# Performance work log

Measured on AMD Instinct MI355X. Metric: run time of the kernel, lower is better.

The kernel has to match this reference:

```python
import jax, jax.numpy as jnp
import numpy as np

NUM_OPS = 8
D = 1024
B = 8192


def setup_inputs() -> dict:
    key = jax.random.key(0)
    k1, k2, k3, k4 = jax.random.split(key, 4)
    x = jax.random.normal(k1, (B, D), dtype=jnp.float32)
    logits = 0.001 * jax.random.normal(k2, (NUM_OPS,), dtype=jnp.float32)
    Ws = jax.random.normal(k3, (NUM_OPS, D, D), dtype=jnp.float32) * (1.0 / np.sqrt(D))
    bs = jax.random.normal(k4, (NUM_OPS, D), dtype=jnp.float32) * 0.01
    return {"x": x, "logits": logits, "Ws": Ws, "bs": bs, "num_on_samples": 2}


def reference(x, logits, Ws, bs, num_on_samples):
    # non_stochastic_call: top-k op selection by architecture logits,
    # dispatch x to the selected ops, sum-combine the results.
    _, top_k_ids = jax.lax.top_k(logits, num_on_samples)  # [k]
    W_sel = jnp.take(Ws, top_k_ids, axis=0)  # [k, D, D]
    b_sel = jnp.take(bs, top_k_ids, axis=0)  # [k, D]
    # each op is Dense(D->D) + relu: [k, B, D]
    op_results = jax.nn.relu(jnp.einsum('bd,kde->kbe', x, W_sel) + b_sel[:, None, :])
    return jnp.sum(op_results, axis=0)  # [B, D]
```

## Files before the change

### kernel.cpp

```cpp
#include <hip/hip_runtime.h>
#include <hip/hip_bf16.h>

#define NUM_OPS 8
#define D 1024
#define B_ROWS 8192

typedef unsigned short ushort_t;
typedef __attribute__((ext_vector_type(8))) short bf16x8;
typedef __attribute__((ext_vector_type(4))) float f32x4;
typedef __attribute__((ext_vector_type(4))) float float4v;
typedef __attribute__((ext_vector_type(8))) unsigned short ushort8;

__device__ __forceinline__ unsigned short f2bf(float f) {
    union { float f; unsigned int u; } v; v.f = f;
    unsigned int u = v.u;
    unsigned int lsb = (u >> 16) & 1u;
    u += 0x7fffu + lsb;
    return (unsigned short)(u >> 16);
}

__device__ __forceinline__ void load_lds16(const void* g, void* l) {
    __builtin_amdgcn_global_load_lds(
        (const __attribute__((address_space(1))) void*)g,
        (__attribute__((address_space(3))) void*)l,
        16, 0, 0);
}

__device__ __forceinline__ void top2(const float* __restrict__ logits, int& i0, int& i1) {
    float best = -__builtin_inff(); i0 = 0;
    for (int i = 0; i < NUM_OPS; ++i) { float v = logits[i]; if (v > best) { best = v; i0 = i; } }
    float best2 = -__builtin_inff(); i1 = 0;
    for (int i = 0; i < NUM_OPS; ++i) {
        if (i == i0) continue;
        float v = logits[i]; if (v > best2) { best2 = v; i1 = i; }
    }
}

__global__ void prep_kernel(const float* __restrict__ x,
                            const float* __restrict__ Ws,
                            const float* __restrict__ logits,
                            ushort_t* __restrict__ xbf,
                            ushort_t* __restrict__ Wt) {
    __shared__ float t[32][33];
    const int bid = blockIdx.x;
    const int tid = threadIdx.x;
    if (bid < 4096) {
        int i = (bid * 256 + tid) * 8;
        float4v v0 = *(const float4v*)(x + i);
        float4v v1 = *(const float4v*)(x + i + 4);
        ushort8 o;
        o[0] = f2bf(v0[0]); o[1] = f2bf(v0[1]); o[2] = f2bf(v0[2]); o[3] = f2bf(v0[3]);
        o[4] = f2bf(v1[0]); o[5] = f2bf(v1[1]); o[6] = f2bf(v1[2]); o[7] = f2bf(v1[3]);
        *(ushort8*)(xbf + i) = o;
    } else {
        int i0, i1; top2(logits, i0, i1);
        const int b  = bid - 4096;
        const int e    = b >> 10;
        const int tile = b & 1023;
        const int td = (tile >> 5) << 5;
        const int te = (tile & 31) << 5;
        const int tx = tid & 31, ty = tid >> 5;
        const float* W = Ws + (size_t)(e ? i1 : i0) * D * D;
        for (int r = 0; r < 4; ++r)
            t[ty + 8 * r][tx] = W[(size_t)(td + ty + 8 * r) * D + te + tx];
        __syncthreads();
        ushort_t* o = Wt + (size_t)e * D * D;
        for (int r = 0; r < 4; ++r)
            o[(size_t)(te + ty + 8 * r) * D + td + tx] = f2bf(t[tx][ty + 8 * r]);
    }
}

__device__ __forceinline__ void stageA(const ushort_t* __restrict__ xbf, int brow,
                                       int u, ushort_t* dst, int tid) {
    #pragma unroll
    for (int q = 0; q < 4; ++q) {
        const int c   = q * 512 + tid;
        const int rr  = c >> 3;
        const int gcb = ((c & 7) * 16) ^ ((rr & 7) << 4);
        load_lds16(xbf + (size_t)(brow + rr) * D + u * 64 + (gcb >> 1), dst + c * 8);
    }
}
__device__ __forceinline__ void stageB(const ushort_t* __restrict__ Wt, int bcol,
                                       int u, ushort_t* dst, int tid) {
    #pragma unroll
    for (int q = 0; q < 2; ++q) {
        const int c   = q * 512 + tid;
        const int e   = c >> 9, cc = c & 511;
        const int n   = cc >> 3;
        const int gcb = ((cc & 7) * 16) ^ ((n & 7) << 4);
        load_lds16(Wt + (size_t)e * D * D + (size_t)(bcol + n) * D + u * 64 + (gcb >> 1),
                   dst + c * 8);
    }
}

#define SB()    __builtin_amdgcn_sched_barrier(0)
#define PRIO1() __builtin_amdgcn_s_setprio(1)
#define PRIO0() __builtin_amdgcn_s_setprio(0)
#define VMW(N)  do { asm volatile("s_waitcnt vmcnt(" #N ")" ::: "memory"); SB(); } while (0)
#define LGW(N)  do { asm volatile("s_waitcnt lgkmcnt(" #N ")" ::: "memory"); SB(); } while (0)
#define BAR()   do { __builtin_amdgcn_s_barrier(); SB(); } while (0)

#define DSR(dst, addr, imm)                                                    \
    asm volatile("ds_read_b128 %0, %1 offset:" #imm : "=v"(dst) : "v"(addr))

#define ISSUE_DS(P, SA, SBB)                                                   \
    do {                                                                       \
        unsigned aA0 = (unsigned)(size_t)(SA) + aro + x0;                      \
        unsigned aA1 = (unsigned)(size_t)(SA) + aro + x1;                      \
        unsigned aB0 = (unsigned)(size_t)(SBB) + bro + x0;                     \
        unsigned aB1 = (unsigned)(size_t)(SBB) + bro + x1;                     \
        DSR(P##a0, aA0, 0);    DSR(P##a1, aA0, 2048);                          \
        DSR(P##a2, aA0, 4096); DSR(P##a3, aA0, 6144);                          \
        DSR(P##a4, aA1, 0);    DSR(P##a5, aA1, 2048);                          \
        DSR(P##a6, aA1, 4096); DSR(P##a7, aA1, 6144);                          \
        DSR(P##b0, aB0, 0);    DSR(P##b1, aB0, 2048);                          \
        DSR(P##b4, aB0, 8192); DSR(P##b5, aB0, 10240);                         \
        DSR(P##b2, aB1, 0);    DSR(P##b3, aB1, 2048);                          \
        DSR(P##b6, aB1, 8192); DSR(P##b7, aB1, 10240);                         \
    } while (0)

#define MF(a, b, c) __builtin_amdgcn_mfma_f32_16x16x32_bf16(a, b, c, 0, 0, 0)
#define Q(P, A, B, E, M, N) acc[E][M][N] = MF(P##A, P##B, acc[E][M][N])

#define MFMA_SET(P)                                                            \
    do {                                                                       \
        PRIO1();                                                               \
        Q(P,a0,b0,0,0,0); Q(P,a0,b1,0,0,1); Q(P,a0,b4,1,0,0); Q(P,a0,b5,1,0,1);\
        Q(P,a1,b0,0,1,0); Q(P,a1,b1,0,1,1); Q(P,a1,b4,1,1,0); Q(P,a1,b5,1,1,1);\
        Q(P,a2,b0,0,2,0); Q(P,a2,b1,0,2,1); Q(P,a2,b4,1,2,0); Q(P,a2,b5,1,2,1);\
        Q(P,a3,b0,0,3,0); Q(P,a3,b1,0,3,1); Q(P,a3,b4,1,3,0); Q(P,a3,b5,1,3,1);\
        Q(P,a4,b2,0,0,0); Q(P,a4,b3,0,0,1); Q(P,a4,b6,1,0,0); Q(P,a4,b7,1,0,1);\
        Q(P,a5,b2,0,1,0); Q(P,a5,b3,0,1,1); Q(P,a5,b6,1,1,0); Q(P,a5,b7,1,1,1);\
        Q(P,a6,b2,0,2,0); Q(P,a6,b3,0,2,1); Q(P,a6,b6,1,2,0); Q(P,a6,b7,1,2,1);\
        Q(P,a7,b2,0,3,0); Q(P,a7,b3,0,3,1); Q(P,a7,b6,1,3,0); Q(P,a7,b7,1,3,1);\
        PRIO0();                                                               \
    } while (0)

#define TILE(SETN, SA, SBB, SU, DA, DB, SETC, DOSTG)                           \
    do {                                                                       \
        VMW(0);                                                                \
        BAR();                                                                 \
        ISSUE_DS(SETN, SA, SBB);                                               \
        if (DOSTG) { stageA(xbf, brow, (SU), DA, tid);                         \
                     stageB(Wt,  bcol, (SU), DB, tid); }                       \
        SB();                                                                  \
        LGW(15);                                                               \
        MFMA_SET(SETC);                                                        \
        SB();                                                                  \
    } while (0)

__global__ __launch_bounds__(512, 2)
void gemm_dual(const ushort_t* __restrict__ xbf, const ushort_t* __restrict__ Wt,
               const float* __restrict__ bs, const float* __restrict__ logits,
               float* __restrict__ out) {
    __shared__ __align__(16) ushort_t As0[256 * 64], As1[256 * 64], As2[256 * 64];
    __shared__ __align__(16) ushort_t Bs0[2 * 64 * 64], Bs1[2 * 64 * 64], Bs2[2 * 64 * 64];

    const int tid  = threadIdx.x;
    const int wv   = tid >> 6;
    const int lane = tid & 63;
    const int rgrp = wv >> 1, cgrp = wv & 1;
    const int l15  = lane & 15, lq = lane >> 4;
    const int swz  = (l15 & 7) << 4;
    const int x0   = (lq * 16) ^ swz;
    const int x1   = (64 + lq * 16) ^ swz;
    const unsigned aro = (unsigned)((rgrp * 64 + l15) * 128);
    const unsigned bro = (unsigned)((cgrp * 32 + l15) * 128);

    const int bid  = blockIdx.x;
    const int brow = (bid & 31) * 256;
    const int bcol = (bid >> 5) * 64;

    f32x4 acc[2][4][2] = {};

    bf16x8 Xa0, Xa1, Xa2, Xa3, Xa4, Xa5, Xa6, Xa7;
    bf16x8 Xb0, Xb1, Xb2, Xb3, Xb4, Xb5, Xb6, Xb7;
    bf16x8 Ya0, Ya1, Ya2, Ya3, Ya4, Ya5, Ya6, Ya7;
    bf16x8 Yb0, Yb1, Yb2, Yb3, Yb4, Yb5, Yb6, Yb7;

    stageA(xbf, brow, 0, As0, tid); stageB(Wt, bcol, 0, Bs0, tid);
    stageA(xbf, brow, 1, As1, tid); stageB(Wt, bcol, 1, Bs1, tid);
    SB();
    VMW(6);
    BAR();
    ISSUE_DS(X, As0, Bs0);
    SB();

    TILE(Y, As1, Bs1,  2, As2, Bs2, X, true);
    TILE(X, As2, Bs2,  3, As0, Bs0, Y, true);
    TILE(Y, As0, Bs0,  4, As1, Bs1, X, true);
    TILE(X, As1, Bs1,  5, As2, Bs2, Y, true);
    TILE(Y, As2, Bs2,  6, As0, Bs0, X, true);
    TILE(X, As0, Bs0,  7, As1, Bs1, Y, true);
    TILE(Y, As1, Bs1,  8, As2, Bs2, X, true);
    TILE(X, As2, Bs2,  9, As0, Bs0, Y, true);
    TILE(Y, As0, Bs0, 10, As1, Bs1, X, true);
    TILE(X, As1, Bs1, 11, As2, Bs2, Y, true);
    TILE(Y, As2, Bs2, 12, As0, Bs0, X, true);
    TILE(X, As0, Bs0, 13, As1, Bs1, Y, true);
    TILE(Y, As1, Bs1, 14, As2, Bs2, X, true);
    TILE(X, As2, Bs2, 15, As0, Bs0, Y, true);
    TILE(Y, As0, Bs0,  0, As0, Bs0, X, false);
    LGW(0);
    MFMA_SET(Y);
    SB();

    int i0, i1; top2(logits, i0, i1);
    #pragma unroll
    for (int n16 = 0; n16 < 2; ++n16) {
        const int col = bcol + cgrp * 32 + n16 * 16 + l15;
        const float bb0 = bs[i0 * D + col];
        const float bb1 = bs[i1 * D + col];
        #pragma unroll
        for (int m = 0; m < 4; ++m) {
            const int rbase = brow + rgrp * 64 + m * 16 + lq * 4;
            #pragma unroll
            for (int i = 0; i < 4; ++i) {
                float v0 = acc[0][m][n16][i] + bb0; v0 = v0 > 0.f ? v0 : 0.f;
                float v1 = acc[1][m][n16][i] + bb1; v1 = v1 > 0.f ? v1 : 0.f;
                out[(size_t)(rbase + i) * D + col] = v0 + v1;
            }
        }
    }
}

extern "C" void kernel_launch(void* const* d_in, const int* in_sizes, int n_in,
                              void* d_out, int out_size, void* d_ws, size_t ws_size,
                              hipStream_t stream) {
    const float* x      = (const float*)d_in[0];
    const float* logits = (const float*)d_in[1];
    const float* Ws     = (const float*)d_in[2];
    const float* bs     = (const float*)d_in[3];
    float* out = (float*)d_out;

    char* ws = (char*)d_ws;
    ushort_t* xbf = (ushort_t*)ws;
    ushort_t* Wt  = (ushort_t*)(ws + (size_t)B_ROWS * D * 2);

    prep_kernel<<<4096 + 2048, 256, 0, stream>>>(x, Ws, logits, xbf, Wt);
    gemm_dual<<<512, 512, 0, stream>>>(xbf, Wt, bs, logits, out);
}
```

Before: 49.06 us.

## Deepen global-to-LDS prefetch to two tiles ahead with partial vmcnt waits

Prologue now stages three K-tiles instead of two. Each iteration waits only until the next tile's loads have landed (vmcnt 6) instead of draining all outstanding loads. The new global loads are issued after the LDS reads have completed, into the buffer those reads just freed. This keeps two tiles of global loads in flight to hide memory latency, in exchange for a tighter buffer-reuse ordering that relies on the barrier placement being correct.

```diff
diff --git a/kernel.cpp b/kernel.cpp
--- a/kernel.cpp
+++ b/kernel.cpp
@@ -136,15 +136,16 @@
         PRIO0();                                                               \
     } while (0)
 
-#define TILE(SETN, SA, SBB, SU, DA, DB, SETC, DOSTG)                           \
+#define TILE(SETN, SA, SBB, SU, DA, DB, SETC, DOSTG, VN)                       \
     do {                                                                       \
-        VMW(0);                                                                \
+        VMW(VN);                                                               \
         BAR();                                                                 \
         ISSUE_DS(SETN, SA, SBB);                                               \
+        SB();                                                                  \
+        LGW(15);                                                               \
         if (DOSTG) { stageA(xbf, brow, (SU), DA, tid);                         \
                      stageB(Wt,  bcol, (SU), DB, tid); }                       \
         SB();                                                                  \
-        LGW(15);                                                               \
         MFMA_SET(SETC);                                                        \
         SB();                                                                  \
     } while (0)
@@ -180,27 +181,28 @@
 
     stageA(xbf, brow, 0, As0, tid); stageB(Wt, bcol, 0, Bs0, tid);
     stageA(xbf, brow, 1, As1, tid); stageB(Wt, bcol, 1, Bs1, tid);
+    stageA(xbf, brow, 2, As2, tid); stageB(Wt, bcol, 2, Bs2, tid);
     SB();
-    VMW(6);
+    VMW(12);
     BAR();
     ISSUE_DS(X, As0, Bs0);
     SB();
 
-    TILE(Y, As1, Bs1,  2, As2, Bs2, X, true);
-    TILE(X, As2, Bs2,  3, As0, Bs0, Y, true);
-    TILE(Y, As0, Bs0,  4, As1, Bs1, X, true);
-    TILE(X, As1, Bs1,  5, As2, Bs2, Y, true);
-    TILE(Y, As2, Bs2,  6, As0, Bs0, X, true);
-    TILE(X, As0, Bs0,  7, As1, Bs1, Y, true);
-    TILE(Y, As1, Bs1,  8, As2, Bs2, X, true);
-    TILE(X, As2, Bs2,  9, As0, Bs0, Y, true);
-    TILE(Y, As0, Bs0, 10, As1, Bs1, X, true);
-    TILE(X, As1, Bs1, 11, As2, Bs2, Y, true);
-    TILE(Y, As2, Bs2, 12, As0, Bs0, X, true);
-    TILE(X, As0, Bs0, 13, As1, Bs1, Y, true);
-    TILE(Y, As1, Bs1, 14, As2, Bs2, X, true);
-    TILE(X, As2, Bs2, 15, As0, Bs0, Y, true);
-    TILE(Y, As0, Bs0,  0, As0, Bs0, X, false);
+    TILE(Y, As1, Bs1,  3, As0, Bs0, X, true,  6);
+    TILE(X, As2, Bs2,  4, As1, Bs1, Y, true,  6);
+    TILE(Y, As0, Bs0,  5, As2, Bs2, X, true,  6);
+    TILE(X, As1, Bs1,  6, As0, Bs0, Y, true,  6);
+    TILE(Y, As2, Bs2,  7, As1, Bs1, X, true,  6);
+    TILE(X, As0, Bs0,  8, As2, Bs2, Y, true,  6);
+    TILE(Y, As1, Bs1,  9, As0, Bs0, X, true,  6);
+    TILE(X, As2, Bs2, 10, As1, Bs1, Y, true,  6);
+    TILE(Y, As0, Bs0, 11, As2, Bs2, X, true,  6);
+    TILE(X, As1, Bs1, 12, As0, Bs0, Y, true,  6);
+    TILE(Y, As2, Bs2, 13, As1, Bs1, X, true,  6);
+    TILE(X, As0, Bs0, 14, As2, Bs2, Y, true,  6);
+    TILE(Y, As1, Bs1, 15, As0, Bs0, X, true,  6);
+    TILE(X, As2, Bs2,  0, As0, Bs0, Y, false, 6);
+    TILE(Y, As0, Bs0,  0, As0, Bs0, X, false, 0);
     LGW(0);
     MFMA_SET(Y);
     SB();
```

Result: faster. 47.07 us, median of 8 (-4.0%).

## Enlarge GEMM tile to 256x128 per expert with simpler double-buffered loop

Applied to the files above, without the earlier changes.

The GEMM block tile grows from 256x64 to 256x128 output columns per expert. Each wave now owns 128 rows by 32 columns, so the accumulators double. The launch drops from 512 to 256 blocks. The hand-scheduled triple-buffered pipeline with inline-asm LDS reads and register ping-pong is replaced by a plain double-buffered loop that relies on the compiler. The aim is more reuse per LDS byte, but it risks higher register pressure, less latency hiding, and only 256 blocks on a 256-CU device with LDS use per block doubled.

```diff
diff --git a/kernel.cpp b/kernel.cpp
--- a/kernel.cpp
+++ b/kernel.cpp
@@ -70,8 +70,8 @@
     }
 }
 
-__device__ __forceinline__ void stageA(const ushort_t* __restrict__ xbf, int brow,
-                                       int u, ushort_t* dst, int tid) {
+__device__ __forceinline__ void stageA2(const ushort_t* __restrict__ xbf, int brow,
+                                        int u, ushort_t* dst, int tid) {
     #pragma unroll
     for (int q = 0; q < 4; ++q) {
         const int c   = q * 512 + tid;
@@ -80,14 +80,14 @@
         load_lds16(xbf + (size_t)(brow + rr) * D + u * 64 + (gcb >> 1), dst + c * 8);
     }
 }
-__device__ __forceinline__ void stageB(const ushort_t* __restrict__ Wt, int bcol,
-                                       int u, ushort_t* dst, int tid) {
+__device__ __forceinline__ void stageB2(const ushort_t* __restrict__ Wt, int bcol,
+                                        int u, ushort_t* dst, int tid) {
     #pragma unroll
-    for (int q = 0; q < 2; ++q) {
+    for (int q = 0; q < 4; ++q) {
         const int c   = q * 512 + tid;
-        const int e   = c >> 9, cc = c & 511;
-        const int n   = cc >> 3;
-        const int gcb = ((cc & 7) * 16) ^ ((n & 7) << 4);
+        const int rr  = c >> 3;
+        const int e   = rr >> 7, n = rr & 127;
+        const int gcb = ((c & 7) * 16) ^ ((rr & 7) << 4);
         load_lds16(Wt + (size_t)e * D * D + (size_t)(bcol + n) * D + u * 64 + (gcb >> 1),
                    dst + c * 8);
     }
@@ -97,113 +97,75 @@
 #define PRIO1() __builtin_amdgcn_s_setprio(1)
 #define PRIO0() __builtin_amdgcn_s_setprio(0)
 #define VMW(N)  do { asm volatile("s_waitcnt vmcnt(" #N ")" ::: "memory"); SB(); } while (0)
-#define LGW(N)  do { asm volatile("s_waitcnt lgkmcnt(" #N ")" ::: "memory"); SB(); } while (0)
 #define BAR()   do { __builtin_amdgcn_s_barrier(); SB(); } while (0)
-
-#define DSR(dst, addr, imm)                                                    \
-    asm volatile("ds_read_b128 %0, %1 offset:" #imm : "=v"(dst) : "v"(addr))
-
-#define ISSUE_DS(P, SA, SBB)                                                   \
-    do {                                                                       \
-        unsigned aA0 = (unsigned)(size_t)(SA) + aro + x0;                      \
-        unsigned aA1 = (unsigned)(size_t)(SA) + aro + x1;                      \
-        unsigned aB0 = (unsigned)(size_t)(SBB) + bro + x0;                     \
-        unsigned aB1 = (unsigned)(size_t)(SBB) + bro + x1;                     \
-        DSR(P##a0, aA0, 0);    DSR(P##a1, aA0, 2048);                          \
-        DSR(P##a2, aA0, 4096); DSR(P##a3, aA0, 6144);                          \
-        DSR(P##a4, aA1, 0);    DSR(P##a5, aA1, 2048);                          \
-        DSR(P##a6, aA1, 4096); DSR(P##a7, aA1, 6144);                          \
-        DSR(P##b0, aB0, 0);    DSR(P##b1, aB0, 2048);                          \
-        DSR(P##b4, aB0, 8192); DSR(P##b5, aB0, 10240);                         \
-        DSR(P##b2, aB1, 0);    DSR(P##b3, aB1, 2048);                          \
-        DSR(P##b6, aB1, 8192); DSR(P##b7, aB1, 10240);                         \
-    } while (0)
-
-#define MF(a, b, c) __builtin_amdgcn_mfma_f32_16x16x32_bf16(a, b, c, 0, 0, 0)
-#define Q(P, A, B, E, M, N) acc[E][M][N] = MF(P##A, P##B, acc[E][M][N])
-
-#define MFMA_SET(P)                                                            \
-    do {                                                                       \
-        PRIO1();                                                               \
-        Q(P,a0,b0,0,0,0); Q(P,a0,b1,0,0,1); Q(P,a0,b4,1,0,0); Q(P,a0,b5,1,0,1);\
-        Q(P,a1,b0,0,1,0); Q(P,a1,b1,0,1,1); Q(P,a1,b4,1,1,0); Q(P,a1,b5,1,1,1);\
-        Q(P,a2,b0,0,2,0); Q(P,a2,b1,0,2,1); Q(P,a2,b4,1,2,0); Q(P,a2,b5,1,2,1);\
-        Q(P,a3,b0,0,3,0); Q(P,a3,b1,0,3,1); Q(P,a3,b4,1,3,0); Q(P,a3,b5,1,3,1);\
-        Q(P,a4,b2,0,0,0); Q(P,a4,b3,0,0,1); Q(P,a4,b6,1,0,0); Q(P,a4,b7,1,0,1);\
-        Q(P,a5,b2,0,1,0); Q(P,a5,b3,0,1,1); Q(P,a5,b6,1,1,0); Q(P,a5,b7,1,1,1);\
-        Q(P,a6,b2,0,2,0); Q(P,a6,b3,0,2,1); Q(P,a6,b6,1,2,0); Q(P,a6,b7,1,2,1);\
-        Q(P,a7,b2,0,3,0); Q(P,a7,b3,0,3,1); Q(P,a7,b6,1,3,0); Q(P,a7,b7,1,3,1);\
-        PRIO0();                                                               \
-    } while (0)
-
-#define TILE(SETN, SA, SBB, SU, DA, DB, SETC, DOSTG)                           \
-    do {                                                                       \
-        VMW(0);                                                                \
-        BAR();                                                                 \
-        ISSUE_DS(SETN, SA, SBB);                                               \
-        if (DOSTG) { stageA(xbf, brow, (SU), DA, tid);                         \
-                     stageB(Wt,  bcol, (SU), DB, tid); }                       \
-        SB();                                                                  \
-        LGW(15);                                                               \
-        MFMA_SET(SETC);                                                        \
-        SB();                                                                  \
-    } while (0)
 
 __global__ __launch_bounds__(512, 2)
 void gemm_dual(const ushort_t* __restrict__ xbf, const ushort_t* __restrict__ Wt,
                const float* __restrict__ bs, const float* __restrict__ logits,
                float* __restrict__ out) {
-    __shared__ __align__(16) ushort_t As0[256 * 64], As1[256 * 64], As2[256 * 64];
-    __shared__ __align__(16) ushort_t Bs0[2 * 64 * 64], Bs1[2 * 64 * 64], Bs2[2 * 64 * 64];
+    __shared__ __align__(16) ushort_t As[2][256 * 64];
+    __shared__ __align__(16) ushort_t Bs[2][256 * 64];
 
     const int tid  = threadIdx.x;
     const int wv   = tid >> 6;
     const int lane = tid & 63;
-    const int rgrp = wv >> 1, cgrp = wv & 1;
+    const int rgrp = wv >> 2;
+    const int cgrp = wv & 3;
     const int l15  = lane & 15, lq = lane >> 4;
     const int swz  = (l15 & 7) << 4;
     const int x0   = (lq * 16) ^ swz;
     const int x1   = (64 + lq * 16) ^ swz;
-    const unsigned aro = (unsigned)((rgrp * 64 + l15) * 128);
-    const unsigned bro = (unsigned)((cgrp * 32 + l15) * 128);
 
     const int bid  = blockIdx.x;
     const int brow = (bid & 31) * 256;
-    const int bcol = (bid >> 5) * 64;
-
-    f32x4 acc[2][4][2] = {};
-
-    bf16x8 Xa0, Xa1, Xa2, Xa3, Xa4, Xa5, Xa6, Xa7;
-    bf16x8 Xb0, Xb1, Xb2, Xb3, Xb4, Xb5, Xb6, Xb7;
-    bf16x8 Ya0, Ya1, Ya2, Ya3, Ya4, Ya5, Ya6, Ya7;
-    bf16x8 Yb0, Yb1, Yb2, Yb3, Yb4, Yb5, Yb6, Yb7;
-
-    stageA(xbf, brow, 0, As0, tid); stageB(Wt, bcol, 0, Bs0, tid);
-    stageA(xbf, brow, 1, As1, tid); stageB(Wt, bcol, 1, Bs1, tid);
-    SB();
-    VMW(6);
-    BAR();
-    ISSUE_DS(X, As0, Bs0);
-    SB();
-
-    TILE(Y, As1, Bs1,  2, As2, Bs2, X, true);
-    TILE(X, As2, Bs2,  3, As0, Bs0, Y, true);
-    TILE(Y, As0, Bs0,  4, As1, Bs1, X, true);
-    TILE(X, As1, Bs1,  5, As2, Bs2, Y, true);
-    TILE(Y, As2, Bs2,  6, As0, Bs0, X, true);
-    TILE(X, As0, Bs0,  7, As1, Bs1, Y, true);
-    TILE(Y, As1, Bs1,  8, As2, Bs2, X, true);
-    TILE(X, As2, Bs2,  9, As0, Bs0, Y, true);
-    TILE(Y, As0, Bs0, 10, As1, Bs1, X, true);
-    TILE(X, As1, Bs1, 11, As2, Bs2, Y, true);
-    TILE(Y, As2, Bs2, 12, As0, Bs0, X, true);
-    TILE(X, As0, Bs0, 13, As1, Bs1, Y, true);
-    TILE(Y, As1, Bs1, 14, As2, Bs2, X, true);
-    TILE(X, As2, Bs2, 15, As0, Bs0, Y, true);
-    TILE(Y, As0, Bs0,  0, As0, Bs0, X, false);
-    LGW(0);
-    MFMA_SET(Y);
-    SB();
+    const int bcol = (bid >> 5) * 128;
+
+    f32x4 acc[2][8][2] = {};
+
+    stageA2(xbf, brow, 0, As[0], tid);
+    stageB2(Wt,  bcol, 0, Bs[0], tid);
+
+    #pragma unroll 1
+    for (int u = 0; u < 16; ++u) {
+        VMW(0);
+        BAR();
+        if (u < 15) {
+            stageA2(xbf, brow, u + 1, As[(u + 1) & 1], tid);
+            stageB2(Wt,  bcol, u + 1, Bs[(u + 1) & 1], tid);
+        }
+        const char* cA = (const char*)As[u & 1];
+        const char* cB = (const char*)Bs[u & 1];
+
+        bf16x8 a[2][8], b[2][2][2];
+        #pragma unroll
+        for (int kk = 0; kk < 2; ++kk)
+            #pragma unroll
+            for (int m = 0; m < 8; ++m)
+                a[kk][m] = *(const bf16x8*)(cA +
+                    (size_t)((rgrp * 128 + m * 16 + l15) * 128) + (kk ? x1 : x0));
+        #pragma unroll
+        for (int e = 0; e < 2; ++e)
+            #pragma unroll
+            for (int kk = 0; kk < 2; ++kk)
+                #pragma unroll
+                for (int n16 = 0; n16 < 2; ++n16)
+                    b[e][kk][n16] = *(const bf16x8*)(cB +
+                        (size_t)((e * 128 + cgrp * 32 + n16 * 16 + l15) * 128) +
+                        (kk ? x1 : x0));
+
+        PRIO1();
+        #pragma unroll
+        for (int kk = 0; kk < 2; ++kk)
+            #pragma unroll
+            for (int e = 0; e < 2; ++e)
+                #pragma unroll
+                for (int m = 0; m < 8; ++m)
+                    #pragma unroll
+                    for (int n16 = 0; n16 < 2; ++n16)
+                        acc[e][m][n16] = __builtin_amdgcn_mfma_f32_16x16x32_bf16(
+                            a[kk][m], b[e][kk][n16], acc[e][m][n16], 0, 0, 0);
+        PRIO0();
+    }
 
     int i0, i1; top2(logits, i0, i1);
     #pragma unroll
@@ -212,8 +174,8 @@
         const float bb0 = bs[i0 * D + col];
         const float bb1 = bs[i1 * D + col];
         #pragma unroll
-        for (int m = 0; m < 4; ++m) {
-            const int rbase = brow + rgrp * 64 + m * 16 + lq * 4;
+        for (int m = 0; m < 8; ++m) {
+            const int rbase = brow + rgrp * 128 + m * 16 + lq * 4;
             #pragma unroll
             for (int i = 0; i < 4; ++i) {
                 float v0 = acc[0][m][n16][i] + bb0; v0 = v0 > 0.f ? v0 : 0.f;
@@ -238,5 +200,5 @@
     ushort_t* Wt  = (ushort_t*)(ws + (size_t)B_ROWS * D * 2);
 
     prep_kernel<<<4096 + 2048, 256, 0, stream>>>(x, Ws, logits, xbf, Wt);
-    gemm_dual<<<512, 512, 0, stream>>>(xbf, Wt, bs, logits, out);
-}
+    gemm_dual<<<256, 512, 0, stream>>>(xbf, Wt, bs, logits, out);
+}
```

After: 60.72 us. 23.8% more time.
